# Kernel optimization log

Hardware: AMD Instinct MI355X
Metric: run time of the kernel (lower is better)

Reference implementation:

```python
import jax, jax.numpy as jnp
import numpy as np

C = 256   # descriptor_dim
H = 4     # num_heads
D = C // H  # head_dim = 64
B, N = 8, 2048


def _conv1x1(x, w, b):
    # 1x1 Conv1d == per-position linear over channels: x [B,C,N], w [O,C], b [O]
    return jnp.einsum('oc,bcn->bon', w, x) + b[None, :, None]


def setup_inputs() -> dict:
    key = jax.random.key(0)
    ks = jax.random.split(key, 11)
    s = 1.0 / np.sqrt(C)
    return {
        'query': jax.random.normal(ks[0], (B, C, N), dtype=jnp.float32),
        'key':   jax.random.normal(ks[1], (B, C, N), dtype=jnp.float32),
        'value': jax.random.normal(ks[2], (B, C, N), dtype=jnp.float32),
        'wq': jax.random.normal(ks[3], (C, C), dtype=jnp.float32) * s,
        'bq': jax.random.normal(ks[4], (C,), dtype=jnp.float32) * s,
        'wk': jax.random.normal(ks[5], (C, C), dtype=jnp.float32) * s,
        'bk': jax.random.normal(ks[6], (C,), dtype=jnp.float32) * s,
        'wv': jax.random.normal(ks[7], (C, C), dtype=jnp.float32) * s,
        'bv': jax.random.normal(ks[8], (C,), dtype=jnp.float32) * s,
        'wm': jax.random.normal(ks[9], (C, C), dtype=jnp.float32) * s,
        'bm': jax.random.normal(ks[10], (C,), dtype=jnp.float32) * s,
    }


def reference(query, key, value, wq, bq, wk, bk, wv, bv, wm, bm):
    b = query.shape[0]
    # project then view channels as (head_dim, num_heads) -- matches torch .view order
    q = _conv1x1(query, wq, bq).reshape(b, D, H, -1)   # [B,D,H,N]
    k = _conv1x1(key,   wk, bk).reshape(b, D, H, -1)   # [B,D,H,M]
    v = _conv1x1(value, wv, bv).reshape(b, D, H, -1)   # [B,D,H,M]
    scores = jnp.einsum('bdhn,bdhm->bhnm', q, k) / (D ** 0.5)
    probs = jax.nn.softmax(scores, axis=-1)            # [B,H,N,M]
    out = jnp.einsum('bhnm,bdhm->bdhn', probs, v)      # [B,D,H,N]
    out = out.reshape(b, D * H, -1)                    # [B,C,N]
    return _conv1x1(out, wm, bm)
```

## Files before the change

kernel.cpp:

```cpp
#include <hip/hip_runtime.h>
#include <hip/hip_bf16.h>

typedef float f32x4 __attribute__((ext_vector_type(4)));
typedef __bf16 bf16x8 __attribute__((ext_vector_type(8)));
typedef __bf16 bf16x4 __attribute__((ext_vector_type(4)));

constexpr int B_ = 8, C_ = 256, N_ = 2048, H_ = 4, D_ = 64;
constexpr int BH_ = B_ * H_;
constexpr float LOG2E = 1.44269504088896340736f;

static __device__ __forceinline__ float fast_exp2(float x) {
#if __has_builtin(__builtin_amdgcn_exp2f)
  return __builtin_amdgcn_exp2f(x);
#else
  return exp2f(x);
#endif
}

static __device__ __forceinline__ void* swz(void* base, int row, int cb) {
  return (char*)base + row * 128 + (cb ^ ((row & 7) << 4));
}
static __device__ __forceinline__ const void* swz(const void* base, int row, int cb) {
  return (const char*)base + row * 128 + (cb ^ ((row & 7) << 4));
}

struct W4 {
  const float* s0; const float* s1; const float* s2; const float* s3;
  __bf16* d0; __bf16* d1; __bf16* d2; __bf16* d3;
};

__global__ __launch_bounds__(256) void wcvt_kernel(W4 p) {
  const int m = blockIdx.y;
  const float* src = m == 0 ? p.s0 : m == 1 ? p.s1 : m == 2 ? p.s2 : p.s3;
  __bf16* dst = m == 0 ? p.d0 : m == 1 ? p.d1 : m == 2 ? p.d2 : p.d3;
  const int f = blockIdx.x * 256 + threadIdx.x;
  const int o_blk = f >> 9;
  const int ks = (f >> 6) & 7;
  const int lane = f & 63;
  const int row = o_blk * 16 + (lane & 15);
  const int kbase = ks * 32 + (lane >> 4) * 8;
  bf16x8 v;
  if (m == 3) {
    for (int e = 0; e < 8; e++) {
      const int k = kbase + e;
      const int c = ((k & 63) << 2) | (k >> 6);
      v[e] = (__bf16)src[row * 256 + c];
    }
  } else {
    const int srow = ((row & 63) << 2) | (row >> 6);
    const float* s = src + srow * 256 + kbase;
    float4 a = *(const float4*)s;
    float4 b = *(const float4*)(s + 4);
    v[0] = (__bf16)a.x; v[1] = (__bf16)a.y; v[2] = (__bf16)a.z; v[3] = (__bf16)a.w;
    v[4] = (__bf16)b.x; v[5] = (__bf16)b.y; v[6] = (__bf16)b.z; v[7] = (__bf16)b.w;
  }
  *(bf16x8*)&dst[(size_t)f * 8] = v;
}

__global__ __launch_bounds__(256) void qkv_fused_kernel(
    const float* __restrict__ xq, const float* __restrict__ xk,
    const float* __restrict__ xv, const __bf16* __restrict__ wfq,
    const __bf16* __restrict__ wfk, const __bf16* __restrict__ wfv,
    const float* __restrict__ bq, const float* __restrict__ bk,
    const float* __restrict__ bv, __bf16* __restrict__ oq,
    __bf16* __restrict__ ok, __bf16* __restrict__ ov) {
  __shared__ __bf16 xlds[64][264];

  const int m = blockIdx.x >> 8;
  int inner = blockIdx.x & 255;
  inner = (inner & 7) * 32 + (inner >> 3);
  const int b = inner >> 5, nb = inner & 31;
  const int n0 = nb * 64;

  const float* xf = m == 0 ? xq : m == 1 ? xk : xv;
  const __bf16* wf = m == 0 ? wfq : m == 1 ? wfk : wfv;
  const float* bias = m == 0 ? bq : m == 1 ? bk : bv;
  __bf16* out = m == 0 ? oq : m == 1 ? ok : ov;
  const float scale = m == 0 ? 0.125f * LOG2E : 1.0f;

  const int t = threadIdx.x;
  {
    const int kl = t >> 4;
    const int nl = (t & 15) * 4;
    const float* src = xf + (size_t)b * C_ * N_ + n0 + nl;
    for (int it = 0; it < 16; it++) {
      const int k = it * 16 + kl;
      float4 f = *(const float4*)(src + (size_t)k * N_);
      xlds[nl + 0][k] = (__bf16)f.x;
      xlds[nl + 1][k] = (__bf16)f.y;
      xlds[nl + 2][k] = (__bf16)f.z;
      xlds[nl + 3][k] = (__bf16)f.w;
    }
  }
  __syncthreads();

  const int lane = t & 63, wvv = t >> 6;
  const int wm = wvv >> 1, wn = wvv & 1;
  const int l15 = lane & 15, lg = lane >> 4;

  f32x4 acc[8][2] = {};

  for (int ks = 0; ks < 8; ks++) {
    bf16x8 bfr[2];
    for (int ni = 0; ni < 2; ni++)
      bfr[ni] = *(const bf16x8*)&xlds[wn * 32 + ni * 16 + l15][ks * 32 + lg * 8];
    for (int mi = 0; mi < 8; mi++) {
      bf16x8 af = *(const bf16x8*)&wf[(((size_t)(wm * 8 + mi) * 8 + ks) * 64 + lane) * 8];
      acc[mi][0] = __builtin_amdgcn_mfma_f32_16x16x32_bf16(af, bfr[0], acc[mi][0], 0, 0, 0);
      acc[mi][1] = __builtin_amdgcn_mfma_f32_16x16x32_bf16(af, bfr[1], acc[mi][1], 0, 0, 0);
    }
  }

  for (int mi = 0; mi < 8; mi++) {
    const int h = wm * 2 + (mi >> 2);
    const int d0 = (mi & 3) * 16 + 4 * lg;
    for (int ni = 0; ni < 2; ni++) {
      const int n = n0 + wn * 32 + ni * 16 + l15;
      if (m != 2) {
        bf16x4 o4;
        for (int r = 0; r < 4; r++)
          o4[r] = (__bf16)((acc[mi][ni][r] + bias[((d0 + r) << 2) | h]) * scale);
        *(bf16x4*)&out[((size_t)(b * H_ + h) * N_ + n) * D_ + d0] = o4;
      } else {
        for (int r = 0; r < 4; r++)
          out[((size_t)(b * H_ + h) * D_ + d0 + r) * N_ + n] =
              (__bf16)(acc[mi][ni][r] + bias[((d0 + r) << 2) | h]);
      }
    }
  }
}

__global__ __launch_bounds__(256) void final_proj_kernel(
    const __bf16* __restrict__ xb, const __bf16* __restrict__ wf,
    const float* __restrict__ bias, float* __restrict__ out) {
  const int bid = blockIdx.x;
  const int wid = (bid & 7) * 128 + (bid >> 3);
  const int o_t = wid & 3;
  const int nb = (wid >> 2) & 31;
  const int b = wid >> 7;
  const int o0 = o_t * 64, n0 = nb * 64;
  const int t = threadIdx.x, lane = t & 63;
  const int wvv = t >> 6, wm = wvv >> 1, wn = wvv & 1;
  const int l15 = lane & 15, lg = lane >> 4;
  const int nbase = n0 + wn * 32 + l15;

  f32x4 acc[2][2] = {};

  for (int ks = 0; ks < 8; ks++) {
    bf16x8 af[2];
    for (int mi = 0; mi < 2; mi++)
      af[mi] = *(const bf16x8*)&wf[(((size_t)(o_t * 4 + wm * 2 + mi) * 8 + ks) * 64 + lane) * 8];
    bf16x8 bfr[2];
    for (int ni = 0; ni < 2; ni++)
      bfr[ni] = *(const bf16x8*)&xb[((size_t)b * N_ + nbase + ni * 16) * C_ + ks * 32 + lg * 8];
    for (int mi = 0; mi < 2; mi++)
      for (int ni = 0; ni < 2; ni++)
        acc[mi][ni] = __builtin_amdgcn_mfma_f32_16x16x32_bf16(
            af[mi], bfr[ni], acc[mi][ni], 0, 0, 0);
  }

  for (int mi = 0; mi < 2; mi++) {
    for (int r = 0; r < 4; r++) {
      const int och = o0 + wm * 32 + mi * 16 + 4 * lg + r;
      const float bv_ = bias[och];
      for (int ni = 0; ni < 2; ni++) {
        const int n = n0 + wn * 32 + ni * 16 + l15;
        out[((size_t)b * C_ + och) * N_ + n] = acc[mi][ni][r] + bv_;
      }
    }
  }
}

__global__ __launch_bounds__(256) void attn_kernel(
    const __bf16* __restrict__ qb, const __bf16* __restrict__ kb,
    const __bf16* __restrict__ vtb, __bf16* __restrict__ attout) {
  __shared__ __bf16 kbuf[2][64][64];
  __shared__ __bf16 vtbuf[2][64][64];
  __shared__ __bf16 p_lds[64][64];

  const int t = threadIdx.x, lane = t & 63, wv = t >> 6;
  const int l15 = lane & 15, lg = lane >> 4;

  const int bid = blockIdx.x;
  const int wid = (bid & 7) * 128 + (bid >> 3);
  const int bh = wid >> 5;
  const int qbase = (wid & 31) * 64;

  const __bf16* k_bh = kb + (size_t)bh * N_ * D_;
  const __bf16* vt_bh = vtb + (size_t)bh * D_ * N_;

  const __bf16* qrow = qb + ((size_t)bh * N_ + qbase + wv * 16 + l15) * D_;
  const bf16x8 qf0 = *(const bf16x8*)(qrow + lg * 8);
  const bf16x8 qf1 = *(const bf16x8*)(qrow + 32 + lg * 8);

  const int srow = t >> 2, sce = (t & 3) * 16;

  f32x4 oacc[4] = {};
  f32x4 lacc = {0.f, 0.f, 0.f, 0.f};
  f32x4 s_a[4], s_b[4];
  uint4 pka, pkc, pva, pvc;

  {
    uint4 a = *(const uint4*)(k_bh + (size_t)srow * D_ + sce);
    uint4 c = *(const uint4*)(k_bh + (size_t)srow * D_ + sce + 8);
    uint4 va = *(const uint4*)(vt_bh + (size_t)srow * N_ + sce);
    uint4 vc = *(const uint4*)(vt_bh + (size_t)srow * N_ + sce + 8);
    *(uint4*)swz(&kbuf[0][0][0], srow, sce * 2) = a;
    *(uint4*)swz(&kbuf[0][0][0], srow, sce * 2 + 16) = c;
    *(uint4*)swz(&vtbuf[0][0][0], srow, sce * 2) = va;
    *(uint4*)swz(&vtbuf[0][0][0], srow, sce * 2 + 16) = vc;
    pka = *(const uint4*)(k_bh + (size_t)(64 + srow) * D_ + sce);
    pkc = *(const uint4*)(k_bh + (size_t)(64 + srow) * D_ + sce + 8);
    pva = *(const uint4*)(vt_bh + (size_t)srow * N_ + 64 + sce);
    pvc = *(const uint4*)(vt_bh + (size_t)srow * N_ + 64 + sce + 8);
  }
  __syncthreads();
  __builtin_amdgcn_s_setprio(1);
  for (int ni = 0; ni < 4; ni++) {
    bf16x8 kf0 = *(const bf16x8*)swz(&kbuf[0][0][0], ni * 16 + l15, lg * 16);
    bf16x8 kf1 = *(const bf16x8*)swz(&kbuf[0][0][0], ni * 16 + l15, 64 + lg * 16);
    s_a[ni] = __builtin_amdgcn_mfma_f32_16x16x32_bf16(kf0, qf0, (f32x4){}, 0, 0, 0);
    s_a[ni] = __builtin_amdgcn_mfma_f32_16x16x32_bf16(kf1, qf1, s_a[ni], 0, 0, 0);
  }
  __builtin_amdgcn_s_setprio(0);
  *(uint4*)swz(&kbuf[1][0][0], srow, sce * 2) = pka;
  *(uint4*)swz(&kbuf[1][0][0], srow, sce * 2 + 16) = pkc;
  *(uint4*)swz(&vtbuf[1][0][0], srow, sce * 2) = pva;
  *(uint4*)swz(&vtbuf[1][0][0], srow, sce * 2 + 16) = pvc;
  __syncthreads();

  auto body = [&](f32x4 (&srd)[4], f32x4 (&swr)[4], const int jj) {
    const int P = jj & 1;
    const bool doNext = (jj + 1) < 32;
    const bool doPre = (jj + 2) < 32;

    if (doNext) {
      __builtin_amdgcn_s_setprio(1);
      for (int ni = 0; ni < 4; ni++) {
        bf16x8 kf0 = *(const bf16x8*)swz(&kbuf[P ^ 1][0][0], ni * 16 + l15, lg * 16);
        bf16x8 kf1 = *(const bf16x8*)swz(&kbuf[P ^ 1][0][0], ni * 16 + l15, 64 + lg * 16);
        swr[ni] = __builtin_amdgcn_mfma_f32_16x16x32_bf16(kf0, qf0, (f32x4){}, 0, 0, 0);
        swr[ni] = __builtin_amdgcn_mfma_f32_16x16x32_bf16(kf1, qf1, swr[ni], 0, 0, 0);
      }
      __builtin_amdgcn_s_setprio(0);
    }
    if (doPre) {
      const int jn = (jj + 2) * 64;
      pka = *(const uint4*)(k_bh + (size_t)(jn + srow) * D_ + sce);
      pkc = *(const uint4*)(k_bh + (size_t)(jn + srow) * D_ + sce + 8);
      pva = *(const uint4*)(vt_bh + (size_t)srow * N_ + jn + sce);
      pvc = *(const uint4*)(vt_bh + (size_t)srow * N_ + jn + sce + 8);
    }
    for (int ni = 0; ni < 4; ni++) {
      bf16x4 pk;
      for (int r = 0; r < 4; r++) {
        const float pp = fast_exp2(srd[ni][r]);
        lacc[r] += pp;
        pk[r] = (__bf16)pp;
      }
      *(bf16x4*)swz(&p_lds[0][0], wv * 16 + l15, 32 * ni + 8 * lg) = pk;
    }
    asm volatile("" ::: "memory");
    __builtin_amdgcn_s_setprio(1);
    for (int kk = 0; kk < 2; kk++) {
      bf16x8 pf = *(const bf16x8*)swz(&p_lds[0][0], wv * 16 + l15, 64 * kk + 16 * lg);
      for (int di = 0; di < 4; di++) {
        bf16x8 vf = *(const bf16x8*)swz(&vtbuf[P][0][0], di * 16 + l15, 64 * kk + 16 * lg);
        oacc[di] = __builtin_amdgcn_mfma_f32_16x16x32_bf16(vf, pf, oacc[di], 0, 0, 0);
      }
    }
    __builtin_amdgcn_s_setprio(0);
    __syncthreads();
    if (doPre) {
      *(uint4*)swz(&kbuf[P][0][0], srow, sce * 2) = pka;
      *(uint4*)swz(&kbuf[P][0][0], srow, sce * 2 + 16) = pkc;
      *(uint4*)swz(&vtbuf[P][0][0], srow, sce * 2) = pva;
      *(uint4*)swz(&vtbuf[P][0][0], srow, sce * 2 + 16) = pvc;
    }
    __syncthreads();
  };

  for (int j = 0; j < 32; j += 2) {
    body(s_a, s_b, j);
    body(s_b, s_a, j + 1);
  }

  float lr = lacc[0] + lacc[1] + lacc[2] + lacc[3];
  lr += __shfl_xor(lr, 16);
  lr += __shfl_xor(lr, 32);
  const float inv = 1.f / lr;
  for (int di = 0; di < 4; di++) {
    bf16x4 ov;
    for (int r = 0; r < 4; r++) ov[r] = (__bf16)(oacc[di][r] * inv);
    *(bf16x4*)swz(&p_lds[0][0], wv * 16 + l15, 32 * di + 8 * lg) = ov;
  }
  asm volatile("" ::: "memory");
  {
    const int orow = lane >> 2, oce = (lane & 3) * 16;
    uint4 o0 = *(uint4*)swz(&p_lds[0][0], wv * 16 + orow, oce * 2);
    uint4 o1 = *(uint4*)swz(&p_lds[0][0], wv * 16 + orow, oce * 2 + 16);
    const int b = bh >> 2, h = bh & 3;
    __bf16* dst = attout + ((size_t)b * N_ + qbase + wv * 16 + orow) * C_ + h * 64 + oce;
    *(uint4*)dst = o0;
    *(uint4*)(dst + 8) = o1;
  }
}

extern "C" void kernel_launch(void* const* d_in, const int* in_sizes, int n_in,
                              void* d_out, int out_size, void* d_ws,
                              size_t ws_size, hipStream_t stream) {
  const float* query = (const float*)d_in[0];
  const float* key_ = (const float*)d_in[1];
  const float* value = (const float*)d_in[2];
  const float* wq = (const float*)d_in[3];
  const float* bq = (const float*)d_in[4];
  const float* wk = (const float*)d_in[5];
  const float* bk = (const float*)d_in[6];
  const float* wv = (const float*)d_in[7];
  const float* bv = (const float*)d_in[8];
  const float* wm = (const float*)d_in[9];
  const float* bm = (const float*)d_in[10];

  const size_t per = (size_t)BH_ * N_ * D_;
  __bf16* qb = (__bf16*)d_ws;
  __bf16* kb = qb + per;
  __bf16* vtb = kb + per;
  __bf16* attout = vtb + per;
  __bf16* wfq = attout + per;
  __bf16* wfk = wfq + 65536;
  __bf16* wfv = wfk + 65536;
  __bf16* wfm = wfv + 65536;

  dim3 blk(256);
  W4 wp{wq, wk, wv, wm, wfq, wfk, wfv, wfm};
  wcvt_kernel<<<dim3(32, 4), blk, 0, stream>>>(wp);

  qkv_fused_kernel<<<768, blk, 0, stream>>>(query, key_, value, wfq, wfk, wfv,
                                            bq, bk, bv, qb, kb, vtb);
  attn_kernel<<<1024, blk, 0, stream>>>(qb, kb, vtb, attout);
  final_proj_kernel<<<1024, blk, 0, stream>>>(attout, wfm, bm, (float*)d_out);
}
```

Measured before the change: 110.3 us.

## Rewrite attention with 32x32 MFMA, register-resident P via permlane swap

Each wave now handles 32 query rows using 32x32x16 MFMA instructions. The probability tile goes straight from S accumulators to the PV operand through permlane32_swap, so the P round-trip through LDS is gone. The pipeline drops the one-tile-ahead QK prefetch and keeps a single barrier per iteration. Output is written in per-head [BH,N,D] layout, and the final projection is re-indexed to match. Fewer blocks with more work each trade occupancy and latency hiding for fewer LDS ops and barriers.

```diff
diff --git a/kernel.cpp b/kernel.cpp
--- a/kernel.cpp
+++ b/kernel.cpp
@@ -2,8 +2,10 @@
 #include <hip/hip_bf16.h>
 
 typedef float f32x4 __attribute__((ext_vector_type(4)));
+typedef float f32x16 __attribute__((ext_vector_type(16)));
 typedef __bf16 bf16x8 __attribute__((ext_vector_type(8)));
 typedef __bf16 bf16x4 __attribute__((ext_vector_type(4)));
+typedef unsigned int uint2v __attribute__((ext_vector_type(2)));
 
 constexpr int B_ = 8, C_ = 256, N_ = 2048, H_ = 4, D_ = 64;
 constexpr int BH_ = B_ * H_;
@@ -151,8 +153,10 @@
     for (int mi = 0; mi < 2; mi++)
       af[mi] = *(const bf16x8*)&wf[(((size_t)(o_t * 4 + wm * 2 + mi) * 8 + ks) * 64 + lane) * 8];
     bf16x8 bfr[2];
+    const size_t bh = (size_t)(b * H_ + (ks >> 1));
+    const int d0 = (ks & 1) * 32 + lg * 8;
     for (int ni = 0; ni < 2; ni++)
-      bfr[ni] = *(const bf16x8*)&xb[((size_t)b * N_ + nbase + ni * 16) * C_ + ks * 32 + lg * 8];
+      bfr[ni] = *(const bf16x8*)&xb[(bh * N_ + nbase + ni * 16) * D_ + d0];
     for (int mi = 0; mi < 2; mi++)
       for (int ni = 0; ni < 2; ni++)
         acc[mi][ni] = __builtin_amdgcn_mfma_f32_16x16x32_bf16(
@@ -176,133 +180,142 @@
     const __bf16* __restrict__ vtb, __bf16* __restrict__ attout) {
   __shared__ __bf16 kbuf[2][64][64];
   __shared__ __bf16 vtbuf[2][64][64];
-  __shared__ __bf16 p_lds[64][64];
 
   const int t = threadIdx.x, lane = t & 63, wv = t >> 6;
-  const int l15 = lane & 15, lg = lane >> 4;
+  const int l31 = lane & 31, hi = lane >> 5;
 
   const int bid = blockIdx.x;
-  const int wid = (bid & 7) * 128 + (bid >> 3);
-  const int bh = wid >> 5;
-  const int qbase = (wid & 31) * 64;
+  const int wid = (bid & 7) * 64 + (bid >> 3);
+  const int bh = wid >> 4;
+  const int qn = (wid & 15) * 128 + wv * 32;
 
   const __bf16* k_bh = kb + (size_t)bh * N_ * D_;
   const __bf16* vt_bh = vtb + (size_t)bh * D_ * N_;
 
-  const __bf16* qrow = qb + ((size_t)bh * N_ + qbase + wv * 16 + l15) * D_;
-  const bf16x8 qf0 = *(const bf16x8*)(qrow + lg * 8);
-  const bf16x8 qf1 = *(const bf16x8*)(qrow + 32 + lg * 8);
+  const __bf16* qrow = qb + ((size_t)bh * N_ + qn + l31) * D_;
+  bf16x8 qf[4];
+#pragma unroll
+  for (int i = 0; i < 4; i++) qf[i] = *(const bf16x8*)(qrow + i * 16 + hi * 8);
 
   const int srow = t >> 2, sce = (t & 3) * 16;
 
-  f32x4 oacc[4] = {};
-  f32x4 lacc = {0.f, 0.f, 0.f, 0.f};
-  f32x4 s_a[4], s_b[4];
-  uint4 pka, pkc, pva, pvc;
-
   {
-    uint4 a = *(const uint4*)(k_bh + (size_t)srow * D_ + sce);
-    uint4 c = *(const uint4*)(k_bh + (size_t)srow * D_ + sce + 8);
+    uint4 ka = *(const uint4*)(k_bh + (size_t)srow * D_ + sce);
+    uint4 kc = *(const uint4*)(k_bh + (size_t)srow * D_ + sce + 8);
     uint4 va = *(const uint4*)(vt_bh + (size_t)srow * N_ + sce);
     uint4 vc = *(const uint4*)(vt_bh + (size_t)srow * N_ + sce + 8);
-    *(uint4*)swz(&kbuf[0][0][0], srow, sce * 2) = a;
-    *(uint4*)swz(&kbuf[0][0][0], srow, sce * 2 + 16) = c;
+    *(uint4*)swz(&kbuf[0][0][0], srow, sce * 2) = ka;
+    *(uint4*)swz(&kbuf[0][0][0], srow, sce * 2 + 16) = kc;
     *(uint4*)swz(&vtbuf[0][0][0], srow, sce * 2) = va;
     *(uint4*)swz(&vtbuf[0][0][0], srow, sce * 2 + 16) = vc;
-    pka = *(const uint4*)(k_bh + (size_t)(64 + srow) * D_ + sce);
-    pkc = *(const uint4*)(k_bh + (size_t)(64 + srow) * D_ + sce + 8);
-    pva = *(const uint4*)(vt_bh + (size_t)srow * N_ + 64 + sce);
-    pvc = *(const uint4*)(vt_bh + (size_t)srow * N_ + 64 + sce + 8);
   }
   __syncthreads();
-  __builtin_amdgcn_s_setprio(1);
-  for (int ni = 0; ni < 4; ni++) {
-    bf16x8 kf0 = *(const bf16x8*)swz(&kbuf[0][0][0], ni * 16 + l15, lg * 16);
-    bf16x8 kf1 = *(const bf16x8*)swz(&kbuf[0][0][0], ni * 16 + l15, 64 + lg * 16);
-    s_a[ni] = __builtin_amdgcn_mfma_f32_16x16x32_bf16(kf0, qf0, (f32x4){}, 0, 0, 0);
-    s_a[ni] = __builtin_amdgcn_mfma_f32_16x16x32_bf16(kf1, qf1, s_a[ni], 0, 0, 0);
-  }
-  __builtin_amdgcn_s_setprio(0);
-  *(uint4*)swz(&kbuf[1][0][0], srow, sce * 2) = pka;
-  *(uint4*)swz(&kbuf[1][0][0], srow, sce * 2 + 16) = pkc;
-  *(uint4*)swz(&vtbuf[1][0][0], srow, sce * 2) = pva;
-  *(uint4*)swz(&vtbuf[1][0][0], srow, sce * 2 + 16) = pvc;
-  __syncthreads();
-
-  auto body = [&](f32x4 (&srd)[4], f32x4 (&swr)[4], const int jj) {
-    const int P = jj & 1;
-    const bool doNext = (jj + 1) < 32;
-    const bool doPre = (jj + 2) < 32;
-
-    if (doNext) {
-      __builtin_amdgcn_s_setprio(1);
-      for (int ni = 0; ni < 4; ni++) {
-        bf16x8 kf0 = *(const bf16x8*)swz(&kbuf[P ^ 1][0][0], ni * 16 + l15, lg * 16);
-        bf16x8 kf1 = *(const bf16x8*)swz(&kbuf[P ^ 1][0][0], ni * 16 + l15, 64 + lg * 16);
-        swr[ni] = __builtin_amdgcn_mfma_f32_16x16x32_bf16(kf0, qf0, (f32x4){}, 0, 0, 0);
-        swr[ni] = __builtin_amdgcn_mfma_f32_16x16x32_bf16(kf1, qf1, swr[ni], 0, 0, 0);
-      }
-      __builtin_amdgcn_s_setprio(0);
-    }
-    if (doPre) {
-      const int jn = (jj + 2) * 64;
+
+  f32x16 o0 = {}, o1 = {};
+  float la0 = 0.f, la1 = 0.f, la2 = 0.f, la3 = 0.f;
+  int cur = 0;
+
+  for (int j0 = 0; j0 < N_; j0 += 64) {
+    const int jn = j0 + 64;
+    const bool have = jn < N_;
+    uint4 pka, pkc, pva, pvc;
+    if (have) {
       pka = *(const uint4*)(k_bh + (size_t)(jn + srow) * D_ + sce);
       pkc = *(const uint4*)(k_bh + (size_t)(jn + srow) * D_ + sce + 8);
       pva = *(const uint4*)(vt_bh + (size_t)srow * N_ + jn + sce);
       pvc = *(const uint4*)(vt_bh + (size_t)srow * N_ + jn + sce + 8);
     }
-    for (int ni = 0; ni < 4; ni++) {
-      bf16x4 pk;
-      for (int r = 0; r < 4; r++) {
-        const float pp = fast_exp2(srd[ni][r]);
-        lacc[r] += pp;
-        pk[r] = (__bf16)pp;
+
+    f32x16 s0 = {}, s1 = {};
+    __builtin_amdgcn_s_setprio(1);
+#pragma unroll
+    for (int i = 0; i < 4; i++) {
+      bf16x8 kf = *(const bf16x8*)swz(&kbuf[cur][0][0], l31, i * 32 + hi * 16);
+      s0 = __builtin_amdgcn_mfma_f32_32x32x16_bf16(kf, qf[i], s0, 0, 0, 0);
+    }
+#pragma unroll
+    for (int i = 0; i < 4; i++) {
+      bf16x8 kf = *(const bf16x8*)swz(&kbuf[cur][0][0], 32 + l31, i * 32 + hi * 16);
+      s1 = __builtin_amdgcn_mfma_f32_32x32x16_bf16(kf, qf[i], s1, 0, 0, 0);
+    }
+    __builtin_amdgcn_s_setprio(0);
+
+#pragma unroll
+    for (int sub = 0; sub < 2; sub++) {
+      const f32x16 s = sub ? s1 : s0;
+      float pr[16];
+#pragma unroll
+      for (int r = 0; r < 16; r++) pr[r] = fast_exp2(s[r]);
+      la0 += pr[0] + pr[4] + pr[8] + pr[12];
+      la1 += pr[1] + pr[5] + pr[9] + pr[13];
+      la2 += pr[2] + pr[6] + pr[10] + pr[14];
+      la3 += pr[3] + pr[7] + pr[11] + pr[15];
+      unsigned w[8];
+#pragma unroll
+      for (int g = 0; g < 8; g++) {
+        union { __bf16 h[2]; unsigned u; } cv;
+        cv.h[0] = (__bf16)pr[2 * g];
+        cv.h[1] = (__bf16)pr[2 * g + 1];
+        w[g] = cv.u;
       }
-      *(bf16x4*)swz(&p_lds[0][0], wv * 16 + l15, 32 * ni + 8 * lg) = pk;
-    }
-    asm volatile("" ::: "memory");
-    __builtin_amdgcn_s_setprio(1);
-    for (int kk = 0; kk < 2; kk++) {
-      bf16x8 pf = *(const bf16x8*)swz(&p_lds[0][0], wv * 16 + l15, 64 * kk + 16 * lg);
-      for (int di = 0; di < 4; di++) {
-        bf16x8 vf = *(const bf16x8*)swz(&vtbuf[P][0][0], di * 16 + l15, 64 * kk + 16 * lg);
-        oacc[di] = __builtin_amdgcn_mfma_f32_16x16x32_bf16(vf, pf, oacc[di], 0, 0, 0);
+      uint2v r0 = __builtin_amdgcn_permlane32_swap(w[0], w[2], false, false);
+      uint2v r1 = __builtin_amdgcn_permlane32_swap(w[1], w[3], false, false);
+      uint2v r2 = __builtin_amdgcn_permlane32_swap(w[4], w[6], false, false);
+      uint2v r3 = __builtin_amdgcn_permlane32_swap(w[5], w[7], false, false);
+      union { unsigned u[4]; bf16x8 v; } f0 = {{r0.x, r1.x, r0.y, r1.y}};
+      union { unsigned u[4]; bf16x8 v; } f1 = {{r2.x, r3.x, r2.y, r3.y}};
+      const int scb = sub * 64;
+      __builtin_amdgcn_s_setprio(1);
+      {
+        bf16x8 vf = *(const bf16x8*)swz(&vtbuf[cur][0][0], l31, scb + hi * 16);
+        o0 = __builtin_amdgcn_mfma_f32_32x32x16_bf16(vf, f0.v, o0, 0, 0, 0);
+        vf = *(const bf16x8*)swz(&vtbuf[cur][0][0], l31, scb + 32 + hi * 16);
+        o0 = __builtin_amdgcn_mfma_f32_32x32x16_bf16(vf, f1.v, o0, 0, 0, 0);
+        vf = *(const bf16x8*)swz(&vtbuf[cur][0][0], 32 + l31, scb + hi * 16);
+        o1 = __builtin_amdgcn_mfma_f32_32x32x16_bf16(vf, f0.v, o1, 0, 0, 0);
+        vf = *(const bf16x8*)swz(&vtbuf[cur][0][0], 32 + l31, scb + 32 + hi * 16);
+        o1 = __builtin_amdgcn_mfma_f32_32x32x16_bf16(vf, f1.v, o1, 0, 0, 0);
       }
-    }
-    __builtin_amdgcn_s_setprio(0);
-    __syncthreads();
-    if (doPre) {
-      *(uint4*)swz(&kbuf[P][0][0], srow, sce * 2) = pka;
-      *(uint4*)swz(&kbuf[P][0][0], srow, sce * 2 + 16) = pkc;
-      *(uint4*)swz(&vtbuf[P][0][0], srow, sce * 2) = pva;
-      *(uint4*)swz(&vtbuf[P][0][0], srow, sce * 2 + 16) = pvc;
-    }
-    __syncthreads();
-  };
-
-  for (int j = 0; j < 32; j += 2) {
-    body(s_a, s_b, j);
-    body(s_b, s_a, j + 1);
-  }
-
-  float lr = lacc[0] + lacc[1] + lacc[2] + lacc[3];
-  lr += __shfl_xor(lr, 16);
-  lr += __shfl_xor(lr, 32);
-  const float inv = 1.f / lr;
-  for (int di = 0; di < 4; di++) {
-    bf16x4 ov;
-    for (int r = 0; r < 4; r++) ov[r] = (__bf16)(oacc[di][r] * inv);
-    *(bf16x4*)swz(&p_lds[0][0], wv * 16 + l15, 32 * di + 8 * lg) = ov;
+      __builtin_amdgcn_s_setprio(0);
+    }
+
+    if (have) {
+      const int nxt = cur ^ 1;
+      *(uint4*)swz(&kbuf[nxt][0][0], srow, sce * 2) = pka;
+      *(uint4*)swz(&kbuf[nxt][0][0], srow, sce * 2 + 16) = pkc;
+      *(uint4*)swz(&vtbuf[nxt][0][0], srow, sce * 2) = pva;
+      *(uint4*)swz(&vtbuf[nxt][0][0], srow, sce * 2 + 16) = pvc;
+      __syncthreads();
+    }
+    cur ^= 1;
+  }
+
+  float la = la0 + la1 + la2 + la3;
+  la += __shfl_xor(la, 32);
+  const float inv = 1.f / la;
+
+  __syncthreads();
+  char* ep = (char*)&vtbuf[0][0][0] + wv * 4096;
+#pragma unroll
+  for (int dt = 0; dt < 2; dt++) {
+    const f32x16 o = dt ? o1 : o0;
+#pragma unroll
+    for (int g = 0; g < 4; g++) {
+      bf16x4 o4;
+#pragma unroll
+      for (int j = 0; j < 4; j++) o4[j] = (__bf16)(o[4 * g + j] * inv);
+      *(bf16x4*)swz(ep, l31, dt * 64 + 16 * g + 8 * hi) = o4;
+    }
   }
   asm volatile("" ::: "memory");
   {
-    const int orow = lane >> 2, oce = (lane & 3) * 16;
-    uint4 o0 = *(uint4*)swz(&p_lds[0][0], wv * 16 + orow, oce * 2);
-    uint4 o1 = *(uint4*)swz(&p_lds[0][0], wv * 16 + orow, oce * 2 + 16);
-    const int b = bh >> 2, h = bh & 3;
-    __bf16* dst = attout + ((size_t)b * N_ + qbase + wv * 16 + orow) * C_ + h * 64 + oce;
-    *(uint4*)dst = o0;
-    *(uint4*)(dst + 8) = o1;
+    __bf16* dst = attout + ((size_t)bh * N_ + qn) * D_;
+#pragma unroll
+    for (int i = 0; i < 4; i++) {
+      const int row = i * 8 + (lane >> 3);
+      uint4 v = *(const uint4*)swz(ep, row, (lane & 7) * 16);
+      *(uint4*)((char*)dst + i * 1024 + lane * 16) = v;
+    }
   }
 }
 
@@ -337,6 +350,6 @@
 
   qkv_fused_kernel<<<768, blk, 0, stream>>>(query, key_, value, wfq, wfk, wfv,
                                             bq, bk, bv, qb, kb, vtb);
-  attn_kernel<<<1024, blk, 0, stream>>>(qb, kb, vtb, attout);
+  attn_kernel<<<512, blk, 0, stream>>>(qb, kb, vtb, attout);
   final_proj_kernel<<<1024, blk, 0, stream>>>(attout, wfm, bm, (float*)d_out);
 }
```

After: 105.2 us. 1.05x faster.
